# Optimization experiments

Measured on AMD Instinct MI355X. Metric: run time of the kernel, lower is better.

## Reference

```python
import jax, jax.numpy as jnp
import numpy as np

B, N, E = 8, 50000, 400000
DIMS = [4, 64, 64, 3]
K = 3
EPS = 1e-5
NEG_SLOPE = 0.01


def _gcn_norm(edge_index, num_nodes):
    # TAGConv uses gcn_norm with unit edge weights and add_self_loops=False.
    row, col = edge_index[0], edge_index[1]
    w = jnp.ones(row.shape[0], dtype=jnp.float32)
    deg = jax.ops.segment_sum(w, col, num_segments=num_nodes)  # in-degree at target
    dis = jnp.where(deg > 0, jnp.power(jnp.maximum(deg, 1.0), -0.5), 0.0)
    return dis[row] * dis[col]  # [E]


def _tag_conv(x, W, b, row, col, norm, num_nodes):
    # x: [B, N, Fin]; W: [K+1, Fin, Fout]; b: [Fout]
    out = jnp.einsum('bnf,fg->bng', x, W[0])
    h = x
    for k in range(1, W.shape[0]):
        msg = h[:, row, :] * norm[None, :, None]            # [B, E, Fin] gather
        h = jnp.zeros((x.shape[0], num_nodes, x.shape[2]), x.dtype).at[:, col, :].add(msg)  # scatter-add
        out = out + jnp.einsum('bnf,fg->bng', h, W[k])
    return out + b


def _batchnorm(x2d, gamma, beta):
    # training-mode BatchNorm1d over batch dim (biased variance, eps=1e-5)
    mean = jnp.mean(x2d, axis=0)
    var = jnp.mean(jnp.square(x2d - mean), axis=0)
    return gamma * (x2d - mean) * jax.lax.rsqrt(var + EPS) + beta


def _leaky_relu(x):
    return jnp.where(x >= 0, x, NEG_SLOPE * x)


def setup_inputs() -> dict:
    key = jax.random.key(0)
    ks = jax.random.split(key, 12)
    inp = {}
    inp['x'] = jax.random.normal(ks[0], (B, N, DIMS[0]), dtype=jnp.float32)
    inp['edge_index'] = jax.random.randint(ks[1], (2, E), 0, N, dtype=jnp.int64)
    inp['val_min'] = jax.random.uniform(ks[2], (N, 3), dtype=jnp.float32) - 1.5
    inp['val_max'] = jax.random.uniform(ks[3], (N, 3), dtype=jnp.float32) + 0.5
    for l in range(3):
        fin, fout = DIMS[l], DIMS[l + 1]
        scale = 1.0 / np.sqrt(fin)
        inp[f'W{l}'] = jax.random.uniform(ks[4 + l], (K + 1, fin, fout), minval=-scale, maxval=scale, dtype=jnp.float32)
        inp[f'b{l}'] = jnp.zeros((fout,), jnp.float32)
    for l in range(2):
        inp[f'gamma{l}'] = jnp.ones((N * DIMS[l + 1],), jnp.float32)
        inp[f'beta{l}'] = jnp.zeros((N * DIMS[l + 1],), jnp.float32)
    return inp


def reference(x, edge_index, val_min, val_max, W0, b0, W1, b1, W2, b2,
              gamma0, beta0, gamma1, beta1):
    row, col = edge_index[0], edge_index[1]
    norm = _gcn_norm(edge_index, N)
    Ws = [W0, W1, W2]
    bs = [b0, b1, b2]
    gammas = [gamma0, gamma1]
    betas = [beta0, beta1]
    out = x
    for layer in range(2):  # num_layers - 1 hidden layers
        out = _tag_conv(out, Ws[layer], bs[layer], row, col, norm, N)
        d = DIMS[layer + 1]
        out = _batchnorm(out.reshape(-1, N * d), gammas[layer], betas[layer]).reshape(-1, N, d)
        out = _leaky_relu(out)
    out = _tag_conv(out, Ws[2], bs[2], row, col, norm, N)  # [B, N, 3]
    # non_linearity: gamma = min + (max - min) / (1 + exp(U))
    return val_min[None] + (val_max - val_min)[None] / (1.0 + jnp.exp(out))
```

## Files before the change

### kernel.cpp

```cpp
#include <hip/hip_runtime.h>
#include <math.h>

constexpr int B = 8;
constexpr int N = 50000;
constexpr int E = 400000;
constexpr float BN_EPS = 1e-5f;
constexpr float NEG = 0.01f;


__device__ __forceinline__ unsigned clamp_src(int s) {
    unsigned u = (unsigned)s;
    return (u < (unsigned)N) ? u : 0u;
}

__device__ __forceinline__ unsigned pack_bf16(float a, float b) {
    unsigned ua = __float_as_uint(a);
    unsigned ub = __float_as_uint(b);
    ua = (ua + 0x7FFFu + ((ua >> 16) & 1u)) >> 16;
    ub = (ub + 0x7FFFu + ((ub >> 16) & 1u)) >> 16;
    return (ub << 16) | (ua & 0xFFFFu);
}
__device__ __forceinline__ float unpack_lo(unsigned u) { return __uint_as_float(u << 16); }
__device__ __forceinline__ float unpack_hi(unsigned u) { return __uint_as_float(u & 0xFFFF0000u); }

__device__ __forceinline__ void store_row64_bf(uint4* p, const float acc[64]) {
#pragma unroll
    for (int q = 0; q < 8; ++q) {
        uint4 v;
        v.x = pack_bf16(acc[q * 8 + 0], acc[q * 8 + 1]);
        v.y = pack_bf16(acc[q * 8 + 2], acc[q * 8 + 3]);
        v.z = pack_bf16(acc[q * 8 + 4], acc[q * 8 + 5]);
        v.w = pack_bf16(acc[q * 8 + 6], acc[q * 8 + 7]);
        p[q] = v;
    }
}


__global__ __launch_bounds__(256) void deg_kernel(const int* __restrict__ col, float* __restrict__ deg) {
    int e = blockIdx.x * blockDim.x + threadIdx.x;
    if (e < E) atomicAdd(&deg[clamp_src(col[e])], 1.0f);
}

__global__ __launch_bounds__(256) void scan1_kernel(const float* __restrict__ deg,
                                                    int* __restrict__ part, int* __restrict__ bsum) {
    __shared__ int sm[4];
    int i = blockIdx.x * blockDim.x + threadIdx.x;
    int v = (i < N) ? (int)deg[i] : 0;
    int lane = threadIdx.x & 63, wv = threadIdx.x >> 6;
    int x = v;
#pragma unroll
    for (int off = 1; off < 64; off <<= 1) {
        int t = __shfl_up(x, off);
        if (lane >= off) x += t;
    }
    if (lane == 63) sm[wv] = x;
    __syncthreads();
    int add = 0;
#pragma unroll
    for (int w = 0; w < 4; ++w) if (w < wv) add += sm[w];
    if (i < N) part[i] = x - v + add;
    if (threadIdx.x == blockDim.x - 1) bsum[blockIdx.x] = x + add;
}

__global__ __launch_bounds__(256) void scan2_kernel(const int* __restrict__ bsum, int* __restrict__ boff,
                                                    int nb, int* __restrict__ rowptr) {
    __shared__ int sm[4];
    int i = threadIdx.x;
    int v = (i < nb) ? bsum[i] : 0;
    int lane = i & 63, wv = i >> 6;
    int x = v;
#pragma unroll
    for (int off = 1; off < 64; off <<= 1) {
        int t = __shfl_up(x, off);
        if (lane >= off) x += t;
    }
    if (lane == 63) sm[wv] = x;
    __syncthreads();
    int add = 0;
#pragma unroll
    for (int w = 0; w < 4; ++w) if (w < wv) add += sm[w];
    if (i < nb) boff[i] = x - v + add;
    if (i == 0) rowptr[N] = E;
}

__global__ __launch_bounds__(256) void scan3_kernel(const int* __restrict__ part, const int* __restrict__ boff,
                                                    int* __restrict__ rowptr) {
    int i = blockIdx.x * blockDim.x + threadIdx.x;
    if (i < N) rowptr[i] = part[i] + boff[blockIdx.x];
}

__global__ __launch_bounds__(256) void fill_kernel(const int* __restrict__ row, const int* __restrict__ col,
                                                   const float* __restrict__ deg, const int* __restrict__ rowptr,
                                                   int* __restrict__ cursor, int* __restrict__ csr_src,
                                                   float* __restrict__ csr_w) {
    int e = blockIdx.x * blockDim.x + threadIdx.x;
    if (e >= E) return;
    unsigned r = clamp_src(row[e]), c = clamp_src(col[e]);
    float dr = deg[r], dc = deg[c];
    float w = (dr > 0.f ? rsqrtf(dr) : 0.f) * (dc > 0.f ? rsqrtf(dc) : 0.f);
    unsigned p = (unsigned)(rowptr[c] + atomicAdd(&cursor[c], 1));
    if (p >= (unsigned)E) p = E - 1;
    csr_src[p] = (int)r;
    csr_w[p] = w;
}


template<bool INBF>
__global__ __launch_bounds__(256) void xprop_kernel(const void* __restrict__ xin, const int* __restrict__ rowptr,
                                                    const int* __restrict__ csr_src, const float* __restrict__ csr_w,
                                                    uint2* __restrict__ xout) {
    int b = blockIdx.x & 7;
    int n = (blockIdx.x >> 3) * blockDim.x + threadIdx.x;
    if (n >= N) return;
    float a0 = 0.f, a1 = 0.f, a2 = 0.f, a3 = 0.f;
    int beg = rowptr[n], end = rowptr[n + 1];
    if (beg < 0) beg = 0;
    if (end > E) end = E;
    for (int i = beg; i < end; ++i) {
        unsigned s = clamp_src(csr_src[i]);
        float w = csr_w[i];
        if constexpr (!INBF) {
            float4 v = *((const float4*)xin + (size_t)b * N + s);
            a0 = fmaf(w, v.x, a0); a1 = fmaf(w, v.y, a1);
            a2 = fmaf(w, v.z, a2); a3 = fmaf(w, v.w, a3);
        } else {
            uint2 v = *((const uint2*)xin + (size_t)b * N + s);
            a0 = fmaf(w, unpack_lo(v.x), a0); a1 = fmaf(w, unpack_hi(v.x), a1);
            a2 = fmaf(w, unpack_lo(v.y), a2); a3 = fmaf(w, unpack_hi(v.y), a3);
        }
    }
    uint2 o;
    o.x = pack_bf16(a0, a1);
    o.y = pack_bf16(a2, a3);
    xout[(size_t)b * N + n] = o;
}


__device__ __forceinline__ void load_xv(const float4* __restrict__ x0, const uint2* __restrict__ x1,
                                        const uint2* __restrict__ x2, const uint2* __restrict__ x3,
                                        size_t ro, float xv[16]) {
    float4 v = x0[ro];
    xv[0] = v.x; xv[1] = v.y; xv[2] = v.z; xv[3] = v.w;
    uint2 u1 = x1[ro], u2 = x2[ro], u3 = x3[ro];
    xv[4] = unpack_lo(u1.x); xv[5] = unpack_hi(u1.x); xv[6] = unpack_lo(u1.y); xv[7] = unpack_hi(u1.y);
    xv[8] = unpack_lo(u2.x); xv[9] = unpack_hi(u2.x); xv[10] = unpack_lo(u2.y); xv[11] = unpack_hi(u2.y);
    xv[12] = unpack_lo(u3.x); xv[13] = unpack_hi(u3.x); xv[14] = unpack_lo(u3.y); xv[15] = unpack_hi(u3.y);
}


__global__ __launch_bounds__(256) void build_h1_kernel(const float4* __restrict__ x0, const uint2* __restrict__ x1,
                                                       const uint2* __restrict__ x2, const uint2* __restrict__ x3,
                                                       const float* __restrict__ W0,
                                                       const float* __restrict__ gamma, const float* __restrict__ beta,
                                                       uint4* __restrict__ h1) {
    int gid = blockIdx.x * blockDim.x + threadIdx.x;
    int node = gid >> 6;
    int lane = gid & 63;
    int fg = lane >> 3, b = lane & 7;
    if (node >= N) return;
    size_t ro = (size_t)b * N + node;
    float xv[16];
    load_xv(x0, x1, x2, x3, ro, xv);
    float z[8];
#pragma unroll
    for (int j = 0; j < 8; ++j) z[j] = 0.f;
#pragma unroll
    for (int kf = 0; kf < 16; ++kf) {
        const float* wr = W0 + kf * 64 + fg * 8;
        float4 wa = *(const float4*)wr;
        float4 wb = *(const float4*)(wr + 4);
        float xs = xv[kf];
        z[0] = fmaf(xs, wa.x, z[0]); z[1] = fmaf(xs, wa.y, z[1]);
        z[2] = fmaf(xs, wa.z, z[2]); z[3] = fmaf(xs, wa.w, z[3]);
        z[4] = fmaf(xs, wb.x, z[4]); z[5] = fmaf(xs, wb.y, z[5]);
        z[6] = fmaf(xs, wb.z, z[6]); z[7] = fmaf(xs, wb.w, z[7]);
    }
    const float* gp = gamma + (size_t)node * 64 + fg * 8;
    const float* bp = beta + (size_t)node * 64 + fg * 8;
    float h[8];
#pragma unroll
    for (int j = 0; j < 8; ++j) {
        float v = z[j];
        float s = v, s2 = v * v;
        s += __shfl_xor(s, 1);  s += __shfl_xor(s, 2);  s += __shfl_xor(s, 4);
        s2 += __shfl_xor(s2, 1); s2 += __shfl_xor(s2, 2); s2 += __shfl_xor(s2, 4);
        float mean = s * 0.125f;
        float var = fmaf(-mean, mean, s2 * 0.125f);
        float rs = rsqrtf(var + BN_EPS);
        float o = fmaf(gp[j] * rs, v - mean, bp[j]);
        h[j] = (o >= 0.f) ? o : NEG * o;
    }
    uint4 o;
    o.x = pack_bf16(h[0], h[1]);
    o.y = pack_bf16(h[2], h[3]);
    o.z = pack_bf16(h[4], h[5]);
    o.w = pack_bf16(h[6], h[7]);
    h1[ro * 8 + fg] = o;
}


__device__ __forceinline__ void gather64_bf(const uint4* __restrict__ ub8, int beg, int end,
                                            const int* __restrict__ csr_src, const float* __restrict__ csr_w,
                                            float acc[64]) {
    if (beg < 0) beg = 0;
    if (end > E) end = E;
    for (int i = beg; i < end; ++i) {
        unsigned s = clamp_src(csr_src[i]);
        float w = csr_w[i];
        const uint4* up = ub8 + (size_t)s * 8;
#pragma unroll
        for (int q = 0; q < 8; ++q) {
            uint4 v = up[q];
            acc[q * 8 + 0] = fmaf(w, unpack_lo(v.x), acc[q * 8 + 0]);
            acc[q * 8 + 1] = fmaf(w, unpack_hi(v.x), acc[q * 8 + 1]);
            acc[q * 8 + 2] = fmaf(w, unpack_lo(v.y), acc[q * 8 + 2]);
            acc[q * 8 + 3] = fmaf(w, unpack_hi(v.y), acc[q * 8 + 3]);
            acc[q * 8 + 4] = fmaf(w, unpack_lo(v.z), acc[q * 8 + 4]);
            acc[q * 8 + 5] = fmaf(w, unpack_hi(v.z), acc[q * 8 + 5]);
            acc[q * 8 + 6] = fmaf(w, unpack_lo(v.w), acc[q * 8 + 6]);
            acc[q * 8 + 7] = fmaf(w, unpack_hi(v.w), acc[q * 8 + 7]);
        }
    }
}

__device__ __forceinline__ void dense64_bf(const uint4* __restrict__ hp8, const float* __restrict__ W, float acc[64]) {
#pragma unroll 1
    for (int kk = 0; kk < 4; ++kk) {
        float hreg[16];
        uint4 va = hp8[kk * 2], vb = hp8[kk * 2 + 1];
        hreg[0] = unpack_lo(va.x); hreg[1] = unpack_hi(va.x);
        hreg[2] = unpack_lo(va.y); hreg[3] = unpack_hi(va.y);
        hreg[4] = unpack_lo(va.z); hreg[5] = unpack_hi(va.z);
        hreg[6] = unpack_lo(va.w); hreg[7] = unpack_hi(va.w);
        hreg[8] = unpack_lo(vb.x); hreg[9] = unpack_hi(vb.x);
        hreg[10] = unpack_lo(vb.y); hreg[11] = unpack_hi(vb.y);
        hreg[12] = unpack_lo(vb.z); hreg[13] = unpack_hi(vb.z);
        hreg[14] = unpack_lo(vb.w); hreg[15] = unpack_hi(vb.w);
        const float* Wp = W + kk * 16 * 64;
#pragma unroll
        for (int k = 0; k < 16; ++k) {
            float hv = hreg[k];
#pragma unroll
            for (int c = 0; c < 64; ++c)
                acc[c] = fmaf(hv, Wp[k * 64 + c], acc[c]);
        }
    }
}


template<int MODE>
__global__ __launch_bounds__(256) void hopM_kernel(const uint4* __restrict__ u_in, const int* __restrict__ rowptr,
                                                   const int* __restrict__ csr_src, const float* __restrict__ csr_w,
                                                   const uint4* __restrict__ h1, int b0, int bmask, int bshift,
                                                   const float* __restrict__ Wk, const float* __restrict__ bias,
                                                   uint4* __restrict__ u_out) {
    int bl = blockIdx.x & bmask;
    int n = (blockIdx.x >> bshift) * blockDim.x + threadIdx.x;
    if (n >= N) return;
    float acc[64];
    if constexpr (MODE == 2) {
#pragma unroll
        for (int f = 0; f < 64; ++f) acc[f] = bias[f];
    } else {
#pragma unroll
        for (int f = 0; f < 64; ++f) acc[f] = 0.f;
    }
    if constexpr (MODE > 0)
        gather64_bf(u_in + (size_t)bl * N * 8, rowptr[n], rowptr[n + 1], csr_src, csr_w, acc);
    dense64_bf(h1 + ((size_t)(b0 + bl) * N + n) * 8, Wk, acc);
    store_row64_bf(u_out + ((size_t)bl * N + n) * 8, acc);
}


__global__ __launch_bounds__(256) void bn_project_kernel(const uint4* __restrict__ zlo, const uint4* __restrict__ zhi,
                                                         const float* __restrict__ gamma, const float* __restrict__ beta,
                                                         const float* __restrict__ W2, float* __restrict__ y) {
    int gid = blockIdx.x * blockDim.x + threadIdx.x;
    int node = gid >> 6;
    int lane = gid & 63;
    int fg = lane >> 3, b = lane & 7;
    if (node >= N) return;
    const uint4* zp = (b < 4) ? (zlo + ((size_t)b * N + node) * 8)
                              : (zhi + ((size_t)(b - 4) * N + node) * 8);
    uint4 v = zp[fg];
    float h[8] = {unpack_lo(v.x), unpack_hi(v.x), unpack_lo(v.y), unpack_hi(v.y),
                  unpack_lo(v.z), unpack_hi(v.z), unpack_lo(v.w), unpack_hi(v.w)};
    const float* gp = gamma + (size_t)node * 64 + fg * 8;
    const float* bp = beta + (size_t)node * 64 + fg * 8;
#pragma unroll
    for (int j = 0; j < 8; ++j) {
        float val = h[j];
        float s = val, s2 = val * val;
        s += __shfl_xor(s, 1);  s += __shfl_xor(s, 2);  s += __shfl_xor(s, 4);
        s2 += __shfl_xor(s2, 1); s2 += __shfl_xor(s2, 2); s2 += __shfl_xor(s2, 4);
        float mean = s * 0.125f;
        float var = fmaf(-mean, mean, s2 * 0.125f);
        float rs = rsqrtf(var + BN_EPS);
        float o = fmaf(gp[j] * rs, val - mean, bp[j]);
        h[j] = (o >= 0.f) ? o : NEG * o;
    }
    float p[12];
#pragma unroll
    for (int k = 0; k < 4; ++k) {
#pragma unroll
        for (int c = 0; c < 3; ++c) {
            float s = 0.f;
#pragma unroll
            for (int j = 0; j < 8; ++j)
                s = fmaf(h[j], W2[k * 192 + (fg * 8 + j) * 3 + c], s);
            p[k * 3 + c] = s;
        }
    }
#pragma unroll
    for (int t = 8; t < 64; t <<= 1) {
#pragma unroll
        for (int i = 0; i < 12; ++i)
            p[i] += __shfl_xor(p[i], t);
    }
    if (fg == 0) {
        size_t bn3 = ((size_t)b * N + node) * 3;
#pragma unroll
        for (int k = 0; k < 4; ++k)
#pragma unroll
            for (int c = 0; c < 3; ++c)
                y[(size_t)k * B * N * 3 + bn3 + c] = p[k * 3 + c];
    }
}


__global__ __launch_bounds__(256) void qprop_kernel(const float* __restrict__ vin, const int* __restrict__ rowptr,
                                                    const int* __restrict__ csr_src, const float* __restrict__ csr_w,
                                                    const float* __restrict__ add, float* __restrict__ vout) {
    int b = blockIdx.x & 7;
    int n = (blockIdx.x >> 3) * blockDim.x + threadIdx.x;
    if (n >= N) return;
    float a0 = 0.f, a1 = 0.f, a2 = 0.f;
    int beg = rowptr[n], end = rowptr[n + 1];
    if (beg < 0) beg = 0;
    if (end > E) end = E;
    const float* base = vin + (size_t)b * N * 3;
    for (int i = beg; i < end; ++i) {
        unsigned s = clamp_src(csr_src[i]);
        float w = csr_w[i];
        const float* p = base + (size_t)s * 3;
        a0 = fmaf(w, p[0], a0);
        a1 = fmaf(w, p[1], a1);
        a2 = fmaf(w, p[2], a2);
    }
    const float* ap = add + ((size_t)b * N + n) * 3;
    float* op = vout + ((size_t)b * N + n) * 3;
    op[0] = a0 + ap[0];
    op[1] = a1 + ap[1];
    op[2] = a2 + ap[2];
}

__global__ __launch_bounds__(256) void qfinal_kernel(const float* __restrict__ vin, const int* __restrict__ rowptr,
                                                     const int* __restrict__ csr_src, const float* __restrict__ csr_w,
                                                     const float* __restrict__ y0, const float* __restrict__ b2,
                                                     const float* __restrict__ vmin, const float* __restrict__ vmax,
                                                     float* __restrict__ out) {
    int b = blockIdx.x & 7;
    int n = (blockIdx.x >> 3) * blockDim.x + threadIdx.x;
    if (n >= N) return;
    float a0 = 0.f, a1 = 0.f, a2 = 0.f;
    int beg = rowptr[n], end = rowptr[n + 1];
    if (beg < 0) beg = 0;
    if (end > E) end = E;
    const float* base = vin + (size_t)b * N * 3;
    for (int i = beg; i < end; ++i) {
        unsigned s = clamp_src(csr_src[i]);
        float w = csr_w[i];
        const float* p = base + (size_t)s * 3;
        a0 = fmaf(w, p[0], a0);
        a1 = fmaf(w, p[1], a1);
        a2 = fmaf(w, p[2], a2);
    }
    size_t bn3 = ((size_t)b * N + n) * 3;
    const float* yp = y0 + bn3;
    float g0 = a0 + yp[0] + b2[0];
    float g1 = a1 + yp[1] + b2[1];
    float g2 = a2 + yp[2] + b2[2];
    float mn0 = vmin[n * 3 + 0], mx0 = vmax[n * 3 + 0];
    float mn1 = vmin[n * 3 + 1], mx1 = vmax[n * 3 + 1];
    float mn2 = vmin[n * 3 + 2], mx2 = vmax[n * 3 + 2];
    float* op = out + bn3;
    op[0] = mn0 + (mx0 - mn0) / (1.f + expf(g0));
    op[1] = mn1 + (mx1 - mn1) / (1.f + expf(g1));
    op[2] = mn2 + (mx2 - mn2) / (1.f + expf(g2));
}


extern "C" void kernel_launch(void* const* d_in, const int* in_sizes, int n_in,
                              void* d_out, int out_size, void* d_ws, size_t ws_size,
                              hipStream_t stream) {
    const float* x      = (const float*)d_in[0];
    const int*   ei     = (const int*)d_in[1];
    const int*   rowi   = ei;
    const int*   coli   = ei + E;
    const float* vmin   = (const float*)d_in[2];
    const float* vmax   = (const float*)d_in[3];
    const float* W0     = (const float*)d_in[4];
    const float* W1     = (const float*)d_in[6];
    const float* b1v    = (const float*)d_in[7];
    const float* W2     = (const float*)d_in[8];
    const float* b2v    = (const float*)d_in[9];
    const float* gamma0 = (const float*)d_in[10];
    const float* beta0  = (const float*)d_in[11];
    const float* gamma1 = (const float*)d_in[12];
    const float* beta1  = (const float*)d_in[13];
    float* out = (float*)d_out;

    const size_t BN3  = (size_t)B * N * 3;
    const size_t H1FL = (size_t)B * N * 32;
    const size_t UCFL = (size_t)4 * N * 32;
    const size_t XBFL = (size_t)B * N * 2;

    auto rnd = [](size_t nf) { return (nf + 63) & ~(size_t)63; };
    size_t off = 0;
    auto alloc = [&](size_t nfloats) -> float* {
        float* p = (float*)d_ws + off;
        off += rnd(nfloats);
        return p;
    };
    float* deg     = alloc(N);
    float* csr_w   = alloc(E);
    int*   rowptr  = (int*)alloc(N + 1);
    int*   part    = (int*)alloc(N);
    int*   bsum    = (int*)alloc(256);
    int*   boff    = (int*)alloc(256);
    int*   cursor  = (int*)alloc(N);
    int*   csr_src = (int*)alloc(E);
    float* h1      = alloc(H1FL);

    const size_t avail_fl = ws_size / 4;
    const size_t need_full = off + 2 * H1FL + 4096;
    bool full = (avail_fl >= need_full);

    float *uA, *uB, *uC = nullptr;
    if (full) {
        uA = alloc(H1FL);
        uB = alloc(H1FL);
    } else {
        uA = alloc(UCFL);
        uB = alloc(UCFL);
        uC = alloc(UCFL);
    }
    uint2* xb1 = (uint2*)uA;
    uint2* xb2 = (uint2*)((float*)uA + XBFL);
    uint2* xb3 = (uint2*)((float*)uA + 2 * XBFL);
    float* y   = h1;
    float* v_a = h1 + rnd(4 * BN3);
    float* v_b = v_a + rnd(BN3);

    const int GE  = (E + 255) / 256;
    const int GN  = (N + 255) / 256;
    const int GB8 = GN * 8;
    const int GH4 = GN * 4;
    const int GW  = (N * 64) / 256;
    dim3 blk(256);

    hipMemsetAsync(deg, 0, N * sizeof(float), stream);
    hipMemsetAsync(cursor, 0, N * sizeof(int), stream);
    deg_kernel<<<GE, blk, 0, stream>>>(coli, deg);
    scan1_kernel<<<GN, blk, 0, stream>>>(deg, part, bsum);
    scan2_kernel<<<1, blk, 0, stream>>>(bsum, boff, GN, rowptr);
    scan3_kernel<<<GN, blk, 0, stream>>>(part, boff, rowptr);
    fill_kernel<<<GE, blk, 0, stream>>>(rowi, coli, deg, rowptr, cursor, csr_src, csr_w);

    xprop_kernel<false><<<GB8, blk, 0, stream>>>(x,   rowptr, csr_src, csr_w, xb1);
    xprop_kernel<true><<<GB8, blk, 0, stream>>>(xb1, rowptr, csr_src, csr_w, xb2);
    xprop_kernel<true><<<GB8, blk, 0, stream>>>(xb2, rowptr, csr_src, csr_w, xb3);
    build_h1_kernel<<<GW, blk, 0, stream>>>((const float4*)x, xb1, xb2, xb3, W0, gamma0, beta0, (uint4*)h1);

    const uint4* H1 = (const uint4*)h1;
    if (full) {
        hopM_kernel<0><<<GB8, blk, 0, stream>>>(nullptr, rowptr, csr_src, csr_w, H1, 0, 7, 3,
                                                W1 + 3 * 4096, nullptr, (uint4*)uA);
        hopM_kernel<1><<<GB8, blk, 0, stream>>>((const uint4*)uA, rowptr, csr_src, csr_w, H1, 0, 7, 3,
                                                W1 + 2 * 4096, nullptr, (uint4*)uB);
        hopM_kernel<1><<<GB8, blk, 0, stream>>>((const uint4*)uB, rowptr, csr_src, csr_w, H1, 0, 7, 3,
                                                W1 + 1 * 4096, nullptr, (uint4*)uA);
        hopM_kernel<2><<<GB8, blk, 0, stream>>>((const uint4*)uA, rowptr, csr_src, csr_w, H1, 0, 7, 3,
                                                W1, b1v, (uint4*)uB);
        bn_project_kernel<<<GW, blk, 0, stream>>>((const uint4*)uB, (const uint4*)(uB + 4 * (size_t)N * 32),
                                                  gamma1, beta1, W2, y);
    } else {
        hopM_kernel<0><<<GB8, blk, 0, stream>>>(nullptr, rowptr, csr_src, csr_w, H1, 0, 7, 3,
                                                W1 + 3 * 4096, nullptr, (uint4*)uA);
        hopM_kernel<1><<<GH4, blk, 0, stream>>>((const uint4*)uA, rowptr, csr_src, csr_w, H1, 0, 3, 2,
                                                W1 + 2 * 4096, nullptr, (uint4*)uC);
        hopM_kernel<1><<<GH4, blk, 0, stream>>>((const uint4*)uC, rowptr, csr_src, csr_w, H1, 0, 3, 2,
                                                W1 + 1 * 4096, nullptr, (uint4*)uA);
        hopM_kernel<2><<<GH4, blk, 0, stream>>>((const uint4*)uA, rowptr, csr_src, csr_w, H1, 0, 3, 2,
                                                W1, b1v, (uint4*)uC);
        hopM_kernel<1><<<GH4, blk, 0, stream>>>((const uint4*)uB, rowptr, csr_src, csr_w, H1, 4, 3, 2,
                                                W1 + 2 * 4096, nullptr, (uint4*)uA);
        hopM_kernel<1><<<GH4, blk, 0, stream>>>((const uint4*)uA, rowptr, csr_src, csr_w, H1, 4, 3, 2,
                                                W1 + 1 * 4096, nullptr, (uint4*)uB);
        hopM_kernel<2><<<GH4, blk, 0, stream>>>((const uint4*)uB, rowptr, csr_src, csr_w, H1, 4, 3, 2,
                                                W1, b1v, (uint4*)uA);
        bn_project_kernel<<<GW, blk, 0, stream>>>((const uint4*)uC, (const uint4*)uA,
                                                  gamma1, beta1, W2, y);
    }

    qprop_kernel<<<GB8, blk, 0, stream>>>(y + 3 * BN3, rowptr, csr_src, csr_w, y + 2 * BN3, v_a);
    qprop_kernel<<<GB8, blk, 0, stream>>>(v_a, rowptr, csr_src, csr_w, y + 1 * BN3, v_b);
    qfinal_kernel<<<GB8, blk, 0, stream>>>(v_b, rowptr, csr_src, csr_w, y, b2v, vmin, vmax, out);
}
```

Measured before the change: 908.6 us.

## Split each node's 64 output features across two threads in hop kernels

The hop kernels now assign two threads per node, each computing 32 of the 64 output channels, which halves the per-thread accumulator array. Launch bounds now request 8 blocks per SM to raise occupancy and latency hiding for the irregular gathers. The cost is duplicated index and weight loads for the edge list and duplicated reads of the dense input row, since each thread still unpacks the full 64-wide h1 row.

```diff
diff --git a/kernel.cpp b/kernel.cpp
--- a/kernel.cpp
+++ b/kernel.cpp
@@ -22,18 +22,6 @@
 }
 __device__ __forceinline__ float unpack_lo(unsigned u) { return __uint_as_float(u << 16); }
 __device__ __forceinline__ float unpack_hi(unsigned u) { return __uint_as_float(u & 0xFFFF0000u); }
-
-__device__ __forceinline__ void store_row64_bf(uint4* p, const float acc[64]) {
-#pragma unroll
-    for (int q = 0; q < 8; ++q) {
-        uint4 v;
-        v.x = pack_bf16(acc[q * 8 + 0], acc[q * 8 + 1]);
-        v.y = pack_bf16(acc[q * 8 + 2], acc[q * 8 + 3]);
-        v.z = pack_bf16(acc[q * 8 + 4], acc[q * 8 + 5]);
-        v.w = pack_bf16(acc[q * 8 + 6], acc[q * 8 + 7]);
-        p[q] = v;
-    }
-}
 
 
 __global__ __launch_bounds__(256) void deg_kernel(const int* __restrict__ col, float* __restrict__ deg) {
@@ -199,17 +187,17 @@
 }
 
 
-__device__ __forceinline__ void gather64_bf(const uint4* __restrict__ ub8, int beg, int end,
+__device__ __forceinline__ void gather32_bf(const uint4* __restrict__ ubase, int beg, int end,
                                             const int* __restrict__ csr_src, const float* __restrict__ csr_w,
-                                            float acc[64]) {
+                                            float acc[32]) {
     if (beg < 0) beg = 0;
     if (end > E) end = E;
     for (int i = beg; i < end; ++i) {
         unsigned s = clamp_src(csr_src[i]);
         float w = csr_w[i];
-        const uint4* up = ub8 + (size_t)s * 8;
-#pragma unroll
-        for (int q = 0; q < 8; ++q) {
+        const uint4* up = ubase + (size_t)s * 8;
+#pragma unroll
+        for (int q = 0; q < 4; ++q) {
             uint4 v = up[q];
             acc[q * 8 + 0] = fmaf(w, unpack_lo(v.x), acc[q * 8 + 0]);
             acc[q * 8 + 1] = fmaf(w, unpack_hi(v.x), acc[q * 8 + 1]);
@@ -223,25 +211,21 @@
     }
 }
 
-__device__ __forceinline__ void dense64_bf(const uint4* __restrict__ hp8, const float* __restrict__ W, float acc[64]) {
+__device__ __forceinline__ void dense32_bf(const uint4* __restrict__ hp8, const float* __restrict__ W, float acc[32]) {
 #pragma unroll 1
-    for (int kk = 0; kk < 4; ++kk) {
-        float hreg[16];
-        uint4 va = hp8[kk * 2], vb = hp8[kk * 2 + 1];
+    for (int kk = 0; kk < 8; ++kk) {
+        uint4 va = hp8[kk];
+        float hreg[8];
         hreg[0] = unpack_lo(va.x); hreg[1] = unpack_hi(va.x);
         hreg[2] = unpack_lo(va.y); hreg[3] = unpack_hi(va.y);
         hreg[4] = unpack_lo(va.z); hreg[5] = unpack_hi(va.z);
         hreg[6] = unpack_lo(va.w); hreg[7] = unpack_hi(va.w);
-        hreg[8] = unpack_lo(vb.x); hreg[9] = unpack_hi(vb.x);
-        hreg[10] = unpack_lo(vb.y); hreg[11] = unpack_hi(vb.y);
-        hreg[12] = unpack_lo(vb.z); hreg[13] = unpack_hi(vb.z);
-        hreg[14] = unpack_lo(vb.w); hreg[15] = unpack_hi(vb.w);
-        const float* Wp = W + kk * 16 * 64;
-#pragma unroll
-        for (int k = 0; k < 16; ++k) {
+        const float* Wp = W + kk * 8 * 64;
+#pragma unroll
+        for (int k = 0; k < 8; ++k) {
             float hv = hreg[k];
 #pragma unroll
-            for (int c = 0; c < 64; ++c)
+            for (int c = 0; c < 32; ++c)
                 acc[c] = fmaf(hv, Wp[k * 64 + c], acc[c]);
         }
     }
@@ -249,26 +233,38 @@
 
 
 template<int MODE>
-__global__ __launch_bounds__(256) void hopM_kernel(const uint4* __restrict__ u_in, const int* __restrict__ rowptr,
-                                                   const int* __restrict__ csr_src, const float* __restrict__ csr_w,
-                                                   const uint4* __restrict__ h1, int b0, int bmask, int bshift,
-                                                   const float* __restrict__ Wk, const float* __restrict__ bias,
-                                                   uint4* __restrict__ u_out) {
+__global__ __launch_bounds__(256, 8) void hopS_kernel(const uint4* __restrict__ u_in, const int* __restrict__ rowptr,
+                                                      const int* __restrict__ csr_src, const float* __restrict__ csr_w,
+                                                      const uint4* __restrict__ h1, int b0, int bmask, int bshift,
+                                                      const float* __restrict__ Wk, const float* __restrict__ bias,
+                                                      uint4* __restrict__ u_out) {
     int bl = blockIdx.x & bmask;
-    int n = (blockIdx.x >> bshift) * blockDim.x + threadIdx.x;
+    int lin = (blockIdx.x >> bshift) * blockDim.x + threadIdx.x;
+    int half = lin & 1;
+    int n = lin >> 1;
     if (n >= N) return;
-    float acc[64];
+    float acc[32];
     if constexpr (MODE == 2) {
-#pragma unroll
-        for (int f = 0; f < 64; ++f) acc[f] = bias[f];
+        const float* bp = bias + half * 32;
+#pragma unroll
+        for (int f = 0; f < 32; ++f) acc[f] = bp[f];
     } else {
 #pragma unroll
-        for (int f = 0; f < 64; ++f) acc[f] = 0.f;
+        for (int f = 0; f < 32; ++f) acc[f] = 0.f;
     }
     if constexpr (MODE > 0)
-        gather64_bf(u_in + (size_t)bl * N * 8, rowptr[n], rowptr[n + 1], csr_src, csr_w, acc);
-    dense64_bf(h1 + ((size_t)(b0 + bl) * N + n) * 8, Wk, acc);
-    store_row64_bf(u_out + ((size_t)bl * N + n) * 8, acc);
+        gather32_bf(u_in + (size_t)bl * N * 8 + half * 4, rowptr[n], rowptr[n + 1], csr_src, csr_w, acc);
+    dense32_bf(h1 + ((size_t)(b0 + bl) * N + n) * 8, Wk + half * 32, acc);
+    uint4* op = u_out + ((size_t)bl * N + n) * 8 + half * 4;
+#pragma unroll
+    for (int q = 0; q < 4; ++q) {
+        uint4 v;
+        v.x = pack_bf16(acc[q * 8 + 0], acc[q * 8 + 1]);
+        v.y = pack_bf16(acc[q * 8 + 2], acc[q * 8 + 3]);
+        v.z = pack_bf16(acc[q * 8 + 4], acc[q * 8 + 5]);
+        v.w = pack_bf16(acc[q * 8 + 6], acc[q * 8 + 7]);
+        op[q] = v;
+    }
 }
 
 
@@ -455,7 +451,7 @@
     const int GE  = (E + 255) / 256;
     const int GN  = (N + 255) / 256;
     const int GB8 = GN * 8;
-    const int GH4 = GN * 4;
+    const int GNH = (2 * N + 255) / 256;
     const int GW  = (N * 64) / 256;
     dim3 blk(256);
 
@@ -474,31 +470,31 @@
 
     const uint4* H1 = (const uint4*)h1;
     if (full) {
-        hopM_kernel<0><<<GB8, blk, 0, stream>>>(nullptr, rowptr, csr_src, csr_w, H1, 0, 7, 3,
-                                                W1 + 3 * 4096, nullptr, (uint4*)uA);
-        hopM_kernel<1><<<GB8, blk, 0, stream>>>((const uint4*)uA, rowptr, csr_src, csr_w, H1, 0, 7, 3,
-                                                W1 + 2 * 4096, nullptr, (uint4*)uB);
-        hopM_kernel<1><<<GB8, blk, 0, stream>>>((const uint4*)uB, rowptr, csr_src, csr_w, H1, 0, 7, 3,
-                                                W1 + 1 * 4096, nullptr, (uint4*)uA);
-        hopM_kernel<2><<<GB8, blk, 0, stream>>>((const uint4*)uA, rowptr, csr_src, csr_w, H1, 0, 7, 3,
-                                                W1, b1v, (uint4*)uB);
+        hopS_kernel<0><<<GNH * 8, blk, 0, stream>>>(nullptr, rowptr, csr_src, csr_w, H1, 0, 7, 3,
+                                                    W1 + 3 * 4096, nullptr, (uint4*)uA);
+        hopS_kernel<1><<<GNH * 8, blk, 0, stream>>>((const uint4*)uA, rowptr, csr_src, csr_w, H1, 0, 7, 3,
+                                                    W1 + 2 * 4096, nullptr, (uint4*)uB);
+        hopS_kernel<1><<<GNH * 8, blk, 0, stream>>>((const uint4*)uB, rowptr, csr_src, csr_w, H1, 0, 7, 3,
+                                                    W1 + 1 * 4096, nullptr, (uint4*)uA);
+        hopS_kernel<2><<<GNH * 8, blk, 0, stream>>>((const uint4*)uA, rowptr, csr_src, csr_w, H1, 0, 7, 3,
+                                                    W1, b1v, (uint4*)uB);
         bn_project_kernel<<<GW, blk, 0, stream>>>((const uint4*)uB, (const uint4*)(uB + 4 * (size_t)N * 32),
                                                   gamma1, beta1, W2, y);
     } else {
-        hopM_kernel<0><<<GB8, blk, 0, stream>>>(nullptr, rowptr, csr_src, csr_w, H1, 0, 7, 3,
-                                                W1 + 3 * 4096, nullptr, (uint4*)uA);
-        hopM_kernel<1><<<GH4, blk, 0, stream>>>((const uint4*)uA, rowptr, csr_src, csr_w, H1, 0, 3, 2,
-                                                W1 + 2 * 4096, nullptr, (uint4*)uC);
-        hopM_kernel<1><<<GH4, blk, 0, stream>>>((const uint4*)uC, rowptr, csr_src, csr_w, H1, 0, 3, 2,
-                                                W1 + 1 * 4096, nullptr, (uint4*)uA);
-        hopM_kernel<2><<<GH4, blk, 0, stream>>>((const uint4*)uA, rowptr, csr_src, csr_w, H1, 0, 3, 2,
-                                                W1, b1v, (uint4*)uC);
-        hopM_kernel<1><<<GH4, blk, 0, stream>>>((const uint4*)uB, rowptr, csr_src, csr_w, H1, 4, 3, 2,
-                                                W1 + 2 * 4096, nullptr, (uint4*)uA);
-        hopM_kernel<1><<<GH4, blk, 0, stream>>>((const uint4*)uA, rowptr, csr_src, csr_w, H1, 4, 3, 2,
-                                                W1 + 1 * 4096, nullptr, (uint4*)uB);
-        hopM_kernel<2><<<GH4, blk, 0, stream>>>((const uint4*)uB, rowptr, csr_src, csr_w, H1, 4, 3, 2,
-                                                W1, b1v, (uint4*)uA);
+        hopS_kernel<0><<<GNH * 8, blk, 0, stream>>>(nullptr, rowptr, csr_src, csr_w, H1, 0, 7, 3,
+                                                    W1 + 3 * 4096, nullptr, (uint4*)uA);
+        hopS_kernel<1><<<GNH * 4, blk, 0, stream>>>((const uint4*)uA, rowptr, csr_src, csr_w, H1, 0, 3, 2,
+                                                    W1 + 2 * 4096, nullptr, (uint4*)uC);
+        hopS_kernel<1><<<GNH * 4, blk, 0, stream>>>((const uint4*)uC, rowptr, csr_src, csr_w, H1, 0, 3, 2,
+                                                    W1 + 1 * 4096, nullptr, (uint4*)uA);
+        hopS_kernel<2><<<GNH * 4, blk, 0, stream>>>((const uint4*)uA, rowptr, csr_src, csr_w, H1, 0, 3, 2,
+                                                    W1, b1v, (uint4*)uC);
+        hopS_kernel<1><<<GNH * 4, blk, 0, stream>>>((const uint4*)uB, rowptr, csr_src, csr_w, H1, 4, 3, 2,
+                                                    W1 + 2 * 4096, nullptr, (uint4*)uA);
+        hopS_kernel<1><<<GNH * 4, blk, 0, stream>>>((const uint4*)uA, rowptr, csr_src, csr_w, H1, 4, 3, 2,
+                                                    W1 + 1 * 4096, nullptr, (uint4*)uB);
+        hopS_kernel<2><<<GNH * 4, blk, 0, stream>>>((const uint4*)uB, rowptr, csr_src, csr_w, H1, 4, 3, 2,
+                                                    W1, b1v, (uint4*)uA);
         bn_project_kernel<<<GW, blk, 0, stream>>>((const uint4*)uC, (const uint4*)uA,
                                                   gamma1, beta1, W2, y);
     }
```

Result: slower. 2.294 ms (+152.5%).
